# Kernel tuning notes

Measured on AMD Instinct MI355X. Metric: run time of the kernel, lower is better.

## Reference

```python
import jax, jax.numpy as jnp
import numpy as np

N_HEAD = 16
N_KV = 4
HEAD_DIM = 128
EPS = float(np.finfo(np.float32).eps)  # torch F.rms_norm default eps


def _rope_tables(T, half, dtype=jnp.float32):
    inv_freq = 1.0 / (10000.0 ** (jnp.arange(half, dtype=dtype) / half))
    ang = jnp.arange(T, dtype=dtype)[:, None] * inv_freq[None, :]  # (T, half)
    cos = jnp.cos(ang)[None, :, None, :]  # (1, T, 1, half)
    sin = jnp.sin(ang)[None, :, None, :]
    return cos, sin


def setup_inputs() -> dict:
    key = jax.random.key(0)
    ks = jax.random.split(key, 5)
    B, T, C = 2, 2048, 2048
    x = jax.random.normal(ks[0], (B, T, C), dtype=jnp.float32)
    cos, sin = _rope_tables(T, HEAD_DIM // 2)
    s = 0.02
    W_Q = jax.random.normal(ks[1], (C, N_HEAD * HEAD_DIM), dtype=jnp.float32) * s
    W_K = jax.random.normal(ks[2], (C, N_KV * HEAD_DIM), dtype=jnp.float32) * s
    W_V = jax.random.normal(ks[3], (C, N_KV * HEAD_DIM), dtype=jnp.float32) * s
    W_O = jax.random.normal(ks[4], (C, C), dtype=jnp.float32) * s
    return {"x": x, "cos": cos, "sin": sin, "W_Q": W_Q, "W_K": W_K, "W_V": W_V, "W_O": W_O}


def _apply_rope(x, cos, sin):
    # x: (B,T,H,D); cos/sin: (1,T,1,D/2)
    d = x.shape[-1] // 2
    x1, x2 = x[..., :d], x[..., d:]
    return jnp.concatenate([x1 * cos + x2 * sin, -x1 * sin + x2 * cos], axis=-1)


def _rms_norm(x):
    return x * jax.lax.rsqrt(jnp.mean(x * x, axis=-1, keepdims=True) + EPS)


def reference(x, cos, sin, W_Q, W_K, W_V, W_O):
    B, T, C = x.shape
    G = N_HEAD // N_KV  # kv groups
    q = (x @ W_Q).reshape(B, T, N_HEAD, HEAD_DIM)
    k = (x @ W_K).reshape(B, T, N_KV, HEAD_DIM)
    v = (x @ W_V).reshape(B, T, N_KV, HEAD_DIM)
    q = _rms_norm(_apply_rope(q, cos[:, :T], sin[:, :T]))
    k = _rms_norm(_apply_rope(k, cos[:, :T], sin[:, :T]))
    # GQA: avoid materializing expanded K/V; group q by kv head
    qg = q.reshape(B, T, N_KV, G, HEAD_DIM)
    scale = 1.0 / jnp.sqrt(jnp.asarray(HEAD_DIM, dtype=x.dtype))
    scores = jnp.einsum("btkgd,bskd->bkgts", qg, k) * scale  # (B,Kv,G,T,T)
    causal = jnp.tril(jnp.ones((T, T), dtype=bool))
    scores = jnp.where(causal, scores, jnp.asarray(-jnp.inf, dtype=scores.dtype))
    attn = jax.nn.softmax(scores, axis=-1)
    out = jnp.einsum("bkgts,bskd->btkgd", attn, v).reshape(B, T, C)
    return out @ W_O
```

## Files before the change

kernel.cpp:

```cpp
#include <hip/hip_runtime.h>
#include <hip/hip_bf16.h>
#include <stdint.h>

typedef __bf16 bf16_4 __attribute__((ext_vector_type(4)));
typedef __bf16 bf16_8 __attribute__((ext_vector_type(8)));
typedef float f32x4 __attribute__((ext_vector_type(4)));

#define AS1 __attribute__((address_space(1)))
#define AS3 __attribute__((address_space(3)))

__device__ __forceinline__ void gload_lds16(const void* g, void* l) {
  __builtin_amdgcn_global_load_lds((const AS1 void*)g, (AS3 void*)l, 16, 0, 0);
}

__device__ __forceinline__ bool is_bf16_mode(const void* cosT) {
  return ((*reinterpret_cast<const uint32_t*>(cosT)) & 0xFFFFu) == 0x3F80u;
}

__global__ __launch_bounds__(256) void prep_all(const void* __restrict__ cosT,
                                                const void* __restrict__ sinT,
                                                const void* __restrict__ x,
                                                const void* __restrict__ WQ,
                                                const void* __restrict__ WK,
                                                const void* __restrict__ WV,
                                                const void* __restrict__ WO,
                                                float* __restrict__ csF,
                                                __bf16* __restrict__ xb,
                                                __bf16* __restrict__ Wt,
                                                __bf16* __restrict__ WOt) {
  const int blk = blockIdx.x, tid = threadIdx.x;
  const bool isb = is_bf16_mode(cosT);
  if (blk < 512) {
    const int i = blk * 256 + tid;
    if (isb) {
      csF[i]          = (float)reinterpret_cast<const __bf16*>(cosT)[i];
      csF[131072 + i] = (float)reinterpret_cast<const __bf16*>(sinT)[i];
    } else {
      csF[i]          = reinterpret_cast<const float*>(cosT)[i];
      csF[131072 + i] = reinterpret_cast<const float*>(sinT)[i];
    }
    return;
  }
  if (blk < 4608) {
    if (isb) return;
    const int i = (blk - 512) * 256 + tid;
    const float4* s = reinterpret_cast<const float4*>(x);
    const float4 a = s[2 * i], c = s[2 * i + 1];
    __bf16 o[8] = {(__bf16)a.x, (__bf16)a.y, (__bf16)a.z, (__bf16)a.w,
                   (__bf16)c.x, (__bf16)c.y, (__bf16)c.z, (__bf16)c.w};
    reinterpret_cast<int4*>(xb)[i] = *reinterpret_cast<int4*>(o);
    return;
  }
  __shared__ __bf16 t[64][33];
  const int tb = blk - 4608;
  const int bx = tb % 160, by = tb / 160;
  const void* src;
  __bf16* dst;
  int C, c0;
  if (bx < 64)      { src = WQ; dst = Wt;                        C = 2048; c0 = bx * 32; }
  else if (bx < 80) { src = WK; dst = Wt + (size_t)2048 * 2048;  C = 512;  c0 = (bx - 64) * 32; }
  else if (bx < 96) { src = WV; dst = Wt + (size_t)2560 * 2048;  C = 512;  c0 = (bx - 80) * 32; }
  else              { src = WO; dst = WOt;                       C = 2048; c0 = (bx - 96) * 32; }
  const int r0 = by * 64;
  {
    const int row = tid >> 2, cb = (tid & 3) * 8;
    bf16_8 v;
    if (isb) {
      v = *reinterpret_cast<const bf16_8*>(
          reinterpret_cast<const __bf16*>(src) + (size_t)(r0 + row) * C + c0 + cb);
    } else {
      const float* sp = reinterpret_cast<const float*>(src) + (size_t)(r0 + row) * C + c0 + cb;
      const float4 a = *reinterpret_cast<const float4*>(sp);
      const float4 b2 = *reinterpret_cast<const float4*>(sp + 4);
      v[0] = (__bf16)a.x;  v[1] = (__bf16)a.y;  v[2] = (__bf16)a.z;  v[3] = (__bf16)a.w;
      v[4] = (__bf16)b2.x; v[5] = (__bf16)b2.y; v[6] = (__bf16)b2.z; v[7] = (__bf16)b2.w;
    }
    #pragma unroll
    for (int k = 0; k < 8; ++k) t[row][cb + k] = v[k];
  }
  __syncthreads();
  {
    const int j = tid >> 3, seg = (tid & 7) * 8;
    bf16_8 v;
    #pragma unroll
    for (int k = 0; k < 8; ++k) v[k] = t[seg + k][j];
    *reinterpret_cast<bf16_8*>(dst + (size_t)(c0 + j) * 2048 + r0 + seg) = v;
  }
}

__global__ __launch_bounds__(512) void gemm8p(const __bf16* __restrict__ A,
                                              const __bf16* __restrict__ Bt,
                                              void* __restrict__ Cv,
                                              int M, int N, int K,
                                              const void* __restrict__ cosRaw) {
  __shared__ __attribute__((aligned(16))) __bf16 As[2][128 * 64];
  __shared__ __attribute__((aligned(16))) __bf16 Bs[2][256 * 64];
  const int tid = threadIdx.x;
  const int lane = tid & 63, w = tid >> 6;
  const int wm = w >> 2, wn = w & 3;
  const int r = lane & 15, g = lane >> 4;
  const int q8 = gridDim.x >> 3;
  const int wg = (blockIdx.x & 7) * q8 + (blockIdx.x >> 3);
  const int gx = M >> 7;
  const int bm = (wg % gx) * 128, bn = (wg / gx) * 256;
  const bool isb = is_bf16_mode(cosRaw);
  const int NT = K >> 6;

  f32x4 acc[4][4] = {};

#define STA(kt, p, j)                                                              \
  {                                                                                \
    const int o_ = tid * 16 + (j) * 8192;                                          \
    const int row_ = o_ >> 7, blk_ = (o_ >> 4) & 7;                                \
    gload_lds16(A + (size_t)(bm + row_) * K + (kt) * 64 + ((blk_ ^ (row_ & 7)) << 3), \
                (char*)As[p] + o_);                                                \
  }
#define STB(kt, p, j)                                                              \
  {                                                                                \
    const int o_ = tid * 16 + (j) * 8192;                                          \
    const int rl_ = o_ >> 7, blk_ = (o_ >> 4) & 7;                                 \
    const int gr_ = ((rl_ >> 5) & 3) * 64 + ((rl_ >> 7) & 1) * 32 + (rl_ & 31);    \
    gload_lds16(Bt + (size_t)(bn + gr_) * K + (kt) * 64 + ((blk_ ^ (rl_ & 7)) << 3), \
                (char*)Bs[p] + o_);                                                \
  }

  STA(0, 0, 0); STA(0, 0, 1);
  STB(0, 0, 0); STB(0, 0, 1); STB(0, 0, 2); STB(0, 0, 3);
  asm volatile("s_waitcnt vmcnt(2)\ns_barrier" ::: "memory");

  for (int kt = 0; kt < NT; ++kt) {
    const int cur = kt & 1, nxt = cur ^ 1;
    const bool pf = (kt + 1 < NT);
    const char* Ac = (const char*)As[cur];
    const char* Bc = (const char*)Bs[cur];

    bf16_8 af[4][2], bf[2][2];
    #pragma unroll
    for (int m = 0; m < 4; ++m)
      #pragma unroll
      for (int kk = 0; kk < 2; ++kk) {
        const int row = wm * 64 + m * 16 + r;
        af[m][kk] = *reinterpret_cast<const bf16_8*>(
            Ac + row * 128 + (((kk * 4 + g) ^ (row & 7)) << 4));
      }
    #pragma unroll
    for (int n = 0; n < 2; ++n)
      #pragma unroll
      for (int kk = 0; kk < 2; ++kk) {
        const int rl = wn * 32 + n * 16 + r;
        bf[n][kk] = *reinterpret_cast<const bf16_8*>(
            Bc + rl * 128 + (((kk * 4 + g) ^ (rl & 7)) << 4));
      }
    if (pf) { STA(kt + 1, nxt, 0); STA(kt + 1, nxt, 1); STB(kt + 1, nxt, 0); }
    __builtin_amdgcn_s_barrier();
    __builtin_amdgcn_s_setprio(1);
    #pragma unroll
    for (int kk = 0; kk < 2; ++kk)
      #pragma unroll
      for (int m = 0; m < 4; ++m)
        #pragma unroll
        for (int n = 0; n < 2; ++n)
          acc[m][n] = __builtin_amdgcn_mfma_f32_16x16x32_bf16(af[m][kk], bf[n][kk], acc[m][n], 0, 0, 0);
    __builtin_amdgcn_s_setprio(0);
    if (pf) asm volatile("s_waitcnt vmcnt(3)\ns_barrier" ::: "memory");
    else    asm volatile("s_waitcnt vmcnt(0)\ns_barrier" ::: "memory");

    bf16_8 bg[2][2];
    #pragma unroll
    for (int n = 0; n < 2; ++n)
      #pragma unroll
      for (int kk = 0; kk < 2; ++kk) {
        const int rl = 128 + wn * 32 + n * 16 + r;
        bg[n][kk] = *reinterpret_cast<const bf16_8*>(
            Bc + rl * 128 + (((kk * 4 + g) ^ (rl & 7)) << 4));
      }
    if (pf) { STB(kt + 1, nxt, 1); STB(kt + 1, nxt, 2); STB(kt + 1, nxt, 3); }
    __builtin_amdgcn_s_barrier();
    __builtin_amdgcn_s_setprio(1);
    #pragma unroll
    for (int kk = 0; kk < 2; ++kk)
      #pragma unroll
      for (int m = 0; m < 4; ++m)
        #pragma unroll
        for (int n = 0; n < 2; ++n)
          acc[m][n + 2] = __builtin_amdgcn_mfma_f32_16x16x32_bf16(af[m][kk], bg[n][kk], acc[m][n + 2], 0, 0, 0);
    __builtin_amdgcn_s_setprio(0);
    if (pf) asm volatile("s_waitcnt vmcnt(2)\ns_barrier" ::: "memory");
    else    asm volatile("s_waitcnt vmcnt(0)\ns_barrier" ::: "memory");
  }
#undef STA
#undef STB

  #pragma unroll
  for (int m = 0; m < 4; ++m)
    #pragma unroll
    for (int n = 0; n < 4; ++n)
      #pragma unroll
      for (int j = 0; j < 4; ++j) {
        const int row = bm + wm * 64 + m * 16 + g * 4 + j;
        const int col = bn + wn * 64 + n * 16 + r;
        const float v = acc[m][n][j];
        if (isb) reinterpret_cast<__bf16*>(Cv)[(size_t)row * N + col] = (__bf16)v;
        else     reinterpret_cast<float*>(Cv)[(size_t)row * N + col] = v;
      }
}

__global__ __launch_bounds__(512) void gemm8p3(const __bf16* __restrict__ Acvt,
                                               const void* __restrict__ Araw,
                                               const __bf16* __restrict__ Bt,
                                               __bf16* __restrict__ Cv,
                                               __bf16* __restrict__ vtOut,
                                               int M, int N, int K,
                                               const void* __restrict__ cosRaw) {
  __shared__ __attribute__((aligned(16))) __bf16 As[2][128 * 64];
  __shared__ __attribute__((aligned(16))) __bf16 Bs[2][384 * 64];
  const int tid = threadIdx.x;
  const int lane = tid & 63, w = tid >> 6;
  const int wm = w >> 2, wn = w & 3;
  const int r = lane & 15, g = lane >> 4;
  const int q8 = gridDim.x >> 3;
  const int wg = (blockIdx.x & 7) * q8 + (blockIdx.x >> 3);
  const int gx = M >> 7;
  const int bm = (wg % gx) * 128, bn = (wg / gx) * 384;
  const int NT = K >> 6;
  const bool isb = is_bf16_mode(cosRaw);
  const __bf16* A = isb ? (const __bf16*)Araw : Acvt;

  f32x4 acc[4][6] = {};

#define STA3(kt, p, j)                                                             \
  {                                                                                \
    const int o_ = tid * 16 + (j) * 8192;                                          \
    const int row_ = o_ >> 7, blk_ = (o_ >> 4) & 7;                                \
    gload_lds16(A + (size_t)(bm + row_) * K + (kt) * 64 + ((blk_ ^ (row_ & 7)) << 3), \
                (char*)As[p] + o_);                                                \
  }
#define STB3(kt, p, j)                                                             \
  {                                                                                \
    const int o_ = tid * 16 + (j) * 8192;                                          \
    const int rl_ = o_ >> 7, blk_ = (o_ >> 4) & 7;                                 \
    const int gr_ = ((rl_ & 127) >> 5) * 96 + (rl_ >> 7) * 32 + (rl_ & 31);        \
    gload_lds16(Bt + (size_t)(bn + gr_) * K + (kt) * 64 + ((blk_ ^ (rl_ & 7)) << 3), \
                (char*)Bs[p] + o_);                                                \
  }

  STA3(0, 0, 0); STA3(0, 0, 1);
  STB3(0, 0, 0); STB3(0, 0, 1); STB3(0, 0, 2);
  STB3(0, 0, 3); STB3(0, 0, 4); STB3(0, 0, 5);
  asm volatile("s_waitcnt vmcnt(4)\ns_barrier" ::: "memory");

  for (int kt = 0; kt < NT; ++kt) {
    const int cur = kt & 1, nxt = cur ^ 1;
    const bool pf = (kt + 1 < NT);
    const char* Ac = (const char*)As[cur];
    const char* Bc = (const char*)Bs[cur];
    bf16_8 af[4][2];

    {
      #pragma unroll
      for (int m = 0; m < 4; ++m)
        #pragma unroll
        for (int kk = 0; kk < 2; ++kk) {
          const int row = wm * 64 + m * 16 + r;
          af[m][kk] = *reinterpret_cast<const bf16_8*>(
              Ac + row * 128 + (((kk * 4 + g) ^ (row & 7)) << 4));
        }
      bf16_8 bf[2][2];
      #pragma unroll
      for (int n = 0; n < 2; ++n)
        #pragma unroll
        for (int kk = 0; kk < 2; ++kk) {
          const int rl = wn * 32 + n * 16 + r;
          bf[n][kk] = *reinterpret_cast<const bf16_8*>(
              Bc + rl * 128 + (((kk * 4 + g) ^ (r & 7)) << 4));
        }
      if (pf) { STA3(kt + 1, nxt, 0); STA3(kt + 1, nxt, 1); STB3(kt + 1, nxt, 0); }
      __builtin_amdgcn_s_barrier();
      __builtin_amdgcn_s_setprio(1);
      #pragma unroll
      for (int kk = 0; kk < 2; ++kk)
        #pragma unroll
        for (int m = 0; m < 4; ++m)
          #pragma unroll
          for (int n = 0; n < 2; ++n)
            acc[m][n] = __builtin_amdgcn_mfma_f32_16x16x32_bf16(af[m][kk], bf[n][kk], acc[m][n], 0, 0, 0);
      __builtin_amdgcn_s_setprio(0);
      if (pf) asm volatile("s_waitcnt vmcnt(5)\ns_barrier" ::: "memory");
      else    asm volatile("s_waitcnt vmcnt(0)\ns_barrier" ::: "memory");
    }

    {
      bf16_8 bf[2][2];
      #pragma unroll
      for (int n = 0; n < 2; ++n)
        #pragma unroll
        for (int kk = 0; kk < 2; ++kk) {
          const int rl = 128 + wn * 32 + n * 16 + r;
          bf[n][kk] = *reinterpret_cast<const bf16_8*>(
              Bc + rl * 128 + (((kk * 4 + g) ^ (r & 7)) << 4));
        }
      if (pf) { STB3(kt + 1, nxt, 1); STB3(kt + 1, nxt, 2); }
      __builtin_amdgcn_s_barrier();
      __builtin_amdgcn_s_setprio(1);
      #pragma unroll
      for (int kk = 0; kk < 2; ++kk)
        #pragma unroll
        for (int m = 0; m < 4; ++m)
          #pragma unroll
          for (int n = 0; n < 2; ++n)
            acc[m][n + 2] = __builtin_amdgcn_mfma_f32_16x16x32_bf16(af[m][kk], bf[n][kk], acc[m][n + 2], 0, 0, 0);
      __builtin_amdgcn_s_setprio(0);
      if (pf) asm volatile("s_waitcnt vmcnt(5)\ns_barrier" ::: "memory");
      else    asm volatile("s_waitcnt vmcnt(0)\ns_barrier" ::: "memory");
    }

    {
      bf16_8 bf[2][2];
      #pragma unroll
      for (int n = 0; n < 2; ++n)
        #pragma unroll
        for (int kk = 0; kk < 2; ++kk) {
          const int rl = 256 + wn * 32 + n * 16 + r;
          bf[n][kk] = *reinterpret_cast<const bf16_8*>(
              Bc + rl * 128 + (((kk * 4 + g) ^ (r & 7)) << 4));
        }
      if (pf) { STB3(kt + 1, nxt, 3); STB3(kt + 1, nxt, 4); STB3(kt + 1, nxt, 5); }
      __builtin_amdgcn_s_barrier();
      __builtin_amdgcn_s_setprio(1);
      #pragma unroll
      for (int kk = 0; kk < 2; ++kk)
        #pragma unroll
        for (int m = 0; m < 4; ++m)
          #pragma unroll
          for (int n = 0; n < 2; ++n)
            acc[m][n + 4] = __builtin_amdgcn_mfma_f32_16x16x32_bf16(af[m][kk], bf[n][kk], acc[m][n + 4], 0, 0, 0);
      __builtin_amdgcn_s_setprio(0);
      if (pf) asm volatile("s_waitcnt vmcnt(4)\ns_barrier" ::: "memory");
      else    asm volatile("s_waitcnt vmcnt(0)\ns_barrier" ::: "memory");
    }
  }
#undef STA3
#undef STB3

  #pragma unroll
  for (int m = 0; m < 4; ++m)
    #pragma unroll
    for (int n = 0; n < 6; ++n) {
      const int row0 = bm + wm * 64 + m * 16 + g * 4;
      const int col  = bn + wn * 96 + n * 16 + r;
      if (isb && col >= 2560) {
        const int vcol = col - 2560;
        const int bb = row0 >> 11;
        const int t0 = row0 & 2047;
        bf16_4 pk;
        #pragma unroll
        for (int j = 0; j < 4; ++j) pk[j] = (__bf16)acc[m][n][j];
        *reinterpret_cast<bf16_4*>(
            &vtOut[((size_t)bb * 512 + vcol) * 2048 + t0]) = pk;
      } else {
        #pragma unroll
        for (int j = 0; j < 4; ++j)
          Cv[(size_t)(row0 + j) * N + col] = (__bf16)acc[m][n][j];
      }
    }
}

__global__ __launch_bounds__(256) void rope_vtrans(__bf16* __restrict__ qkv,
                                                   const float* __restrict__ csF,
                                                   __bf16* __restrict__ vt,
                                                   const void* __restrict__ cosRaw) {
  const int blk = blockIdx.x, tid = threadIdx.x;
  if (blk < 4096) {
    const int gw = blk * 4 + (tid >> 6);
    const int lane = tid & 63;
    const int head = 16 + (gw & 3);
    const int m = gw >> 2;
    const int t = m & 2047;
    __bf16* p = qkv + (size_t)m * 3072 + head * 128;
    const float x1 = (float)p[lane];
    const float x2 = (float)p[lane + 64];
    const float c = csF[t * 64 + lane];
    const float s = csF[131072 + t * 64 + lane];
    const float y1 = x1 * c + x2 * s;
    const float y2 = x2 * c - x1 * s;
    float ss = y1 * y1 + y2 * y2;
    #pragma unroll
    for (int mk = 32; mk >= 1; mk >>= 1) ss += __shfl_xor(ss, mk, 64);
    const float inv = rsqrtf(ss * (1.0f / 128.0f) + 1.1920929e-7f);
    p[lane] = (__bf16)(y1 * inv);
    p[lane + 64] = (__bf16)(y2 * inv);
    return;
  }
  if (is_bf16_mode(cosRaw)) return;
  __shared__ __bf16 t[32][33];
  const int vb = blk - 4096;
  const int z = vb >> 10, rem = vb & 1023;
  const int x = rem & 63, y = rem >> 6;
  const int tx = tid & 31, ty = tid >> 5;
  const int t0 = x * 32, c0 = y * 32;
  #pragma unroll
  for (int i = 0; i < 32; i += 8)
    t[ty + i][tx] = qkv[(size_t)(z * 2048 + t0 + ty + i) * 3072 + 2560 + c0 + tx];
  __syncthreads();
  #pragma unroll
  for (int i = 0; i < 32; i += 8)
    vt[(size_t)(z * 512 + c0 + ty + i) * 2048 + t0 + tx] = t[tx][ty + i];
}

__global__ __launch_bounds__(256) void attn_fwd7(const __bf16* __restrict__ qkv,
                                                 const __bf16* __restrict__ vt,
                                                 __bf16* __restrict__ out,
                                                 const float* __restrict__ csF,
                                                 const void* __restrict__ cosRawT,
                                                 const void* __restrict__ sinRawT) {
  __shared__ __attribute__((aligned(16))) __bf16 Kl[64 * 128];
  __shared__ __attribute__((aligned(16))) __bf16 Vl[128 * 64];
  __shared__ __attribute__((aligned(16))) __bf16 Pl[4][16][64];

  const int tid = threadIdx.x, lane = tid & 63, w = tid >> 6;
  const int r = lane & 15, g = lane >> 4;
  const int lid = blockIdx.x;
  const int grp = lid & 7, inner = lid >> 3;
  const int b = grp >> 2, kvh = grp & 3;
  const int h = kvh * 4 + (inner & 3);
  const int qt = 31 - (inner >> 2);
  const int qpos = qt * 64 + w * 16 + r;
  const __bf16* Kbase = qkv + (size_t)(b * 2048) * 3072 + 2048 + kvh * 128;
  const __bf16* Vbase = vt + (size_t)((b * 4 + kvh) * 128) * 2048;

#define STAGE(kt)                                                               \
  {                                                                             \
    _Pragma("unroll")                                                           \
    for (int i_ = 0; i_ < 4; ++i_) {                                            \
      const int o_ = tid * 16 + i_ * 4096;                                      \
      const int krow_ = o_ >> 8;                                                \
      const int jj_ = (o_ >> 4) & 15;                                           \
      const int gj_ = (jj_ & 8) | ((jj_ ^ krow_) & 7);                          \
      gload_lds16(Kbase + (size_t)((kt) * 64 + krow_) * 3072 + gj_ * 8,         \
                  (char*)Kl + o_);                                              \
      const int d_ = o_ >> 7;                                                   \
      const int j2_ = (o_ >> 4) & 7;                                            \
      const int g2_ = j2_ ^ (d_ & 7);                                           \
      gload_lds16(Vbase + (size_t)d_ * 2048 + (kt) * 64 + g2_ * 8,              \
                  (char*)Vl + o_);                                              \
    }                                                                           \
  }

#define ATTN_TILE(kt, MASKED)                                                   \
  {                                                                             \
    STAGE(kt);                                                                  \
    asm volatile("s_waitcnt vmcnt(0)" ::: "memory");                            \
    __syncthreads();                                                            \
    f32x4 sacc[4] = {};                                                         \
    _Pragma("unroll")                                                           \
    for (int kb = 0; kb < 4; ++kb) {                                            \
      const int jj = kb * 4 + g;                                                \
      const int jp = (jj & 8) | ((jj ^ (r & 7)) & 7);                           \
      _Pragma("unroll")                                                         \
      for (int n = 0; n < 4; ++n) {                                             \
        const bf16_8 kf = *reinterpret_cast<const bf16_8*>(                     \
            (char*)Kl + (n * 16 + r) * 256 + jp * 16);                          \
        sacc[n] = __builtin_amdgcn_mfma_f32_16x16x32_bf16(kf, qf[kb], sacc[n], 0, 0, 0); \
      }                                                                         \
    }                                                                           \
    float p[4][4];                                                              \
    float pm = -1e30f;                                                          \
    _Pragma("unroll")                                                           \
    for (int n = 0; n < 4; ++n)                                                 \
      _Pragma("unroll")                                                         \
      for (int j = 0; j < 4; ++j) {                                             \
        float sv = sacc[n][j];                                                  \
        if (MASKED && ((kt) * 64 + n * 16 + g * 4 + j > qpos)) sv = -1e30f;     \
        p[n][j] = sv;                                                           \
        pm = fmaxf(pm, sv);                                                     \
      }                                                                         \
    pm = fmaxf(pm, __shfl_xor(pm, 16, 64));                                     \
    pm = fmaxf(pm, __shfl_xor(pm, 32, 64));                                     \
    float mn = mst;                                                             \
    if (!__all(pm - mst <= 12.0f)) {                                            \
      mn = fmaxf(mst, pm);                                                      \
      const float alpha = exp2f(mst - mn);                                      \
      mst = mn;                                                                 \
      lst *= alpha;                                                             \
      float av[4];                                                              \
      _Pragma("unroll")                                                         \
      for (int j = 0; j < 4; ++j) av[j] = __shfl(alpha, g * 4 + j, 64);         \
      _Pragma("unroll")                                                         \
      for (int dt = 0; dt < 8; ++dt)                                            \
        _Pragma("unroll")                                                       \
        for (int j = 0; j < 4; ++j) accO[dt][j] *= av[j];                       \
    }                                                                           \
    float rs = 0.0f;                                                            \
    _Pragma("unroll")                                                           \
    for (int n = 0; n < 4; ++n)                                                 \
      _Pragma("unroll")                                                         \
      for (int j = 0; j < 4; ++j) {                                             \
        p[n][j] = exp2f(p[n][j] - mn);                                          \
        rs += p[n][j];                                                          \
      }                                                                         \
    rs += __shfl_xor(rs, 16, 64);                                               \
    rs += __shfl_xor(rs, 32, 64);                                               \
    lst += rs;                                                                  \
    _Pragma("unroll")                                                           \
    for (int n = 0; n < 4; ++n) {                                               \
      bf16_4 pk;                                                                \
      _Pragma("unroll")                                                         \
      for (int j = 0; j < 4; ++j) pk[j] = (__bf16)p[n][j];                      \
      const int blk = 2 * n + (g >> 1);                                         \
      char* pw = plw + r * 128 + ((blk ^ (r & 7)) << 4) + (g & 1) * 8;          \
      *reinterpret_cast<bf16_4*>(pw) = pk;                                      \
    }                                                                           \
    _Pragma("unroll")                                                           \
    for (int half = 0; half < 2; ++half) {                                      \
      const bf16_8 pa = *reinterpret_cast<const bf16_8*>(                       \
          plw + r * 128 + (((half * 4 + g) ^ (r & 7)) << 4));                   \
      _Pragma("unroll")                                                         \
      for (int dt = 0; dt < 8; ++dt) {                                          \
        const int d = dt * 16 + r;                                              \
        const bf16_8 vf = *reinterpret_cast<const bf16_8*>(                     \
            (char*)Vl + d * 128 + ((half * 4 + g) ^ (d & 7)) * 16);             \
        accO[dt] = __builtin_amdgcn_mfma_f32_16x16x32_bf16(pa, vf, accO[dt], 0, 0, 0); \
      }                                                                         \
    }                                                                           \
    __syncthreads();                                                            \
  }

  bf16_8 qf[4];
  {
    const int trow = qt * 64 + w * 16 + r;
    const __bf16* qp = qkv + (size_t)(b * 2048 + trow) * 3072 + h * 128 + g * 8;
    bf16_8 rq[4];
    #pragma unroll
    for (int kb = 0; kb < 4; ++kb) rq[kb] = *reinterpret_cast<const bf16_8*>(qp + kb * 32);
    float cv[16], sv[16];
    if (is_bf16_mode(cosRawT)) {
      const __bf16* cb = reinterpret_cast<const __bf16*>(cosRawT) + (size_t)trow * 64 + g * 8;
      const __bf16* sb = reinterpret_cast<const __bf16*>(sinRawT) + (size_t)trow * 64 + g * 8;
      const bf16_8 clo = *reinterpret_cast<const bf16_8*>(cb);
      const bf16_8 chi = *reinterpret_cast<const bf16_8*>(cb + 32);
      const bf16_8 slo = *reinterpret_cast<const bf16_8*>(sb);
      const bf16_8 shi = *reinterpret_cast<const bf16_8*>(sb + 32);
      #pragma unroll
      for (int i = 0; i < 8; ++i) {
        cv[i] = (float)clo[i];  cv[8 + i] = (float)chi[i];
        sv[i] = (float)slo[i];  sv[8 + i] = (float)shi[i];
      }
    } else {
      const float* cb = csF + (size_t)trow * 64 + g * 8;
      const float* sb = csF + 131072 + (size_t)trow * 64 + g * 8;
      #pragma unroll
      for (int i = 0; i < 2; ++i) {
        const float4 c0 = *reinterpret_cast<const float4*>(cb + i * 4);
        const float4 c1 = *reinterpret_cast<const float4*>(cb + 32 + i * 4);
        const float4 s0 = *reinterpret_cast<const float4*>(sb + i * 4);
        const float4 s1 = *reinterpret_cast<const float4*>(sb + 32 + i * 4);
        cv[i * 4 + 0] = c0.x; cv[i * 4 + 1] = c0.y; cv[i * 4 + 2] = c0.z; cv[i * 4 + 3] = c0.w;
        cv[8 + i * 4 + 0] = c1.x; cv[8 + i * 4 + 1] = c1.y; cv[8 + i * 4 + 2] = c1.z; cv[8 + i * 4 + 3] = c1.w;
        sv[i * 4 + 0] = s0.x; sv[i * 4 + 1] = s0.y; sv[i * 4 + 2] = s0.z; sv[i * 4 + 3] = s0.w;
        sv[8 + i * 4 + 0] = s1.x; sv[8 + i * 4 + 1] = s1.y; sv[8 + i * 4 + 2] = s1.z; sv[8 + i * 4 + 3] = s1.w;
      }
    }
    float y[4][8];
    float ss = 0.0f;
    #pragma unroll
    for (int i = 0; i < 8; ++i) {
      const float c0 = cv[i],     s0 = sv[i];
      const float c1 = cv[8 + i], s1 = sv[8 + i];
      const float xa0 = (float)rq[0][i], xb0 = (float)rq[2][i];
      const float xa1 = (float)rq[1][i], xb1 = (float)rq[3][i];
      y[0][i] = xa0 * c0 + xb0 * s0;
      y[2][i] = xb0 * c0 - xa0 * s0;
      y[1][i] = xa1 * c1 + xb1 * s1;
      y[3][i] = xb1 * c1 - xa1 * s1;
      ss += y[0][i] * y[0][i] + y[1][i] * y[1][i] + y[2][i] * y[2][i] + y[3][i] * y[3][i];
    }
    ss += __shfl_xor(ss, 16, 64);
    ss += __shfl_xor(ss, 32, 64);
    const float inv = rsqrtf(ss * (1.0f / 128.0f) + 1.1920929e-7f) * 0.12751743f;
    #pragma unroll
    for (int kb = 0; kb < 4; ++kb)
      #pragma unroll
      for (int i = 0; i < 8; ++i) qf[kb][i] = (__bf16)(y[kb][i] * inv);
  }

  char* const plw = (char*)Pl + w * 2048;
  f32x4 accO[8] = {};
  float mst = -1e30f, lst = 0.0f;

  for (int kt = 0; kt < qt; ++kt) ATTN_TILE(kt, false);
  ATTN_TILE(qt, true);

  float lv[4];
  #pragma unroll
  for (int j = 0; j < 4; ++j) lv[j] = 1.0f / __shfl(lst, g * 4 + j, 64);
  #pragma unroll
  for (int dt = 0; dt < 8; ++dt)
    #pragma unroll
    for (int j = 0; j < 4; ++j) {
      const int t = qt * 64 + w * 16 + g * 4 + j;
      out[(size_t)(b * 2048 + t) * 2048 + h * 128 + dt * 16 + r] = (__bf16)(accO[dt][j] * lv[j]);
    }
#undef ATTN_TILE
#undef STAGE
}

extern "C" void kernel_launch(void* const* d_in, const int* in_sizes, int n_in,
                              void* d_out, int out_size, void* d_ws, size_t ws_size,
                              hipStream_t stream) {
  const void* x    = d_in[0];
  const void* cosT = d_in[1];
  const void* sinT = d_in[2];
  const void* W_Q  = d_in[3];
  const void* W_K  = d_in[4];
  const void* W_V  = d_in[5];
  const void* W_O  = d_in[6];

  const int B = 2, T = 2048, C = 2048;
  const int M = B * T;
  const int NQKV = 3072;

  char* ws = (char*)d_ws;
  ws += 256;
  float*  csF  = (float*)ws;                     ws += (size_t)2 * 131072 * 4;
  __bf16* xb   = (__bf16*)ws;                    ws += (size_t)M * C * 2;
  __bf16* Wt   = (__bf16*)ws;                    ws += (size_t)NQKV * C * 2;
  __bf16* WOt  = (__bf16*)ws;                    ws += (size_t)C * C * 2;
  __bf16* QKV  = (__bf16*)ws;                    ws += (size_t)M * NQKV * 2;
  __bf16* AO   = (__bf16*)ws;                    ws += (size_t)M * C * 2;
  __bf16* VT   = xb;

  prep_all<<<dim3(9728), 256, 0, stream>>>(cosT, sinT, x, W_Q, W_K, W_V, W_O,
                                           csF, xb, Wt, WOt);
  gemm8p3<<<dim3((M / 128) * (NQKV / 384)), 512, 0, stream>>>(xb, x, Wt, QKV, VT, M, NQKV, C, cosT);
  rope_vtrans<<<dim3(6144), 256, 0, stream>>>(QKV, csF, VT, cosT);
  attn_fwd7<<<dim3(1024), 256, 0, stream>>>(QKV, VT, AO, csF, cosT, sinT);
  gemm8p<<<dim3((M / 128) * (C / 256)), 512, 0, stream>>>(AO, WOt, d_out, M, C, C, cosT);
}
```

Measured before the change: 194.2 us.

## Double-buffer K/V tiles in attention to overlap global loads with compute

The attention kernel now keeps two LDS buffers for the K and V tiles. It issues the asynchronous global-to-LDS load for tile kt+1 before computing tile kt, and uses a partial vmcnt wait plus raw barriers instead of a full drain and __syncthreads each iteration. The goal is to hide global memory latency behind the MFMA and softmax work. In exchange, LDS use roughly doubles (about 72KB per block), which may lower occupancy, and correctness now depends on the hand-written waitcnt and barrier ordering.

```diff
diff --git a/kernel.cpp b/kernel.cpp
--- a/kernel.cpp
+++ b/kernel.cpp
@@ -407,14 +407,14 @@
     vt[(size_t)(z * 512 + c0 + ty + i) * 2048 + t0 + tx] = t[tx][ty + i];
 }
 
-__global__ __launch_bounds__(256) void attn_fwd7(const __bf16* __restrict__ qkv,
+__global__ __launch_bounds__(256) void attn_fwd9(const __bf16* __restrict__ qkv,
                                                  const __bf16* __restrict__ vt,
                                                  __bf16* __restrict__ out,
                                                  const float* __restrict__ csF,
                                                  const void* __restrict__ cosRawT,
                                                  const void* __restrict__ sinRawT) {
-  __shared__ __attribute__((aligned(16))) __bf16 Kl[64 * 128];
-  __shared__ __attribute__((aligned(16))) __bf16 Vl[128 * 64];
+  __shared__ __attribute__((aligned(16))) __bf16 Kl[2][64 * 128];
+  __shared__ __attribute__((aligned(16))) __bf16 Vl[2][128 * 64];
   __shared__ __attribute__((aligned(16))) __bf16 Pl[4][16][64];
 
   const int tid = threadIdx.x, lane = tid & 63, w = tid >> 6;
@@ -428,7 +428,7 @@
   const __bf16* Kbase = qkv + (size_t)(b * 2048) * 3072 + 2048 + kvh * 128;
   const __bf16* Vbase = vt + (size_t)((b * 4 + kvh) * 128) * 2048;
 
-#define STAGE(kt)                                                               \
+#define STAGE(kt, p)                                                            \
   {                                                                             \
     _Pragma("unroll")                                                           \
     for (int i_ = 0; i_ < 4; ++i_) {                                            \
@@ -437,20 +437,19 @@
       const int jj_ = (o_ >> 4) & 15;                                           \
       const int gj_ = (jj_ & 8) | ((jj_ ^ krow_) & 7);                          \
       gload_lds16(Kbase + (size_t)((kt) * 64 + krow_) * 3072 + gj_ * 8,         \
-                  (char*)Kl + o_);                                              \
+                  (char*)Kl[p] + o_);                                           \
       const int d_ = o_ >> 7;                                                   \
       const int j2_ = (o_ >> 4) & 7;                                            \
       const int g2_ = j2_ ^ (d_ & 7);                                           \
       gload_lds16(Vbase + (size_t)d_ * 2048 + (kt) * 64 + g2_ * 8,              \
-                  (char*)Vl + o_);                                              \
+                  (char*)Vl[p] + o_);                                           \
     }                                                                           \
   }
 
-#define ATTN_TILE(kt, MASKED)                                                   \
+#define ATTN_TILE(kt, p, MASKED)                                                \
   {                                                                             \
-    STAGE(kt);                                                                  \
-    asm volatile("s_waitcnt vmcnt(0)" ::: "memory");                            \
-    __syncthreads();                                                            \
+    const char* Kc = (const char*)Kl[p];                                        \
+    const char* Vc = (const char*)Vl[p];                                        \
     f32x4 sacc[4] = {};                                                         \
     _Pragma("unroll")                                                           \
     for (int kb = 0; kb < 4; ++kb) {                                            \
@@ -459,11 +458,11 @@
       _Pragma("unroll")                                                         \
       for (int n = 0; n < 4; ++n) {                                             \
         const bf16_8 kf = *reinterpret_cast<const bf16_8*>(                     \
-            (char*)Kl + (n * 16 + r) * 256 + jp * 16);                          \
+            Kc + (n * 16 + r) * 256 + jp * 16);                                 \
         sacc[n] = __builtin_amdgcn_mfma_f32_16x16x32_bf16(kf, qf[kb], sacc[n], 0, 0, 0); \
       }                                                                         \
     }                                                                           \
-    float p[4][4];                                                              \
+    float p_[4][4];                                                             \
     float pm = -1e30f;                                                          \
     _Pragma("unroll")                                                           \
     for (int n = 0; n < 4; ++n)                                                 \
@@ -471,7 +470,7 @@
       for (int j = 0; j < 4; ++j) {                                             \
         float sv = sacc[n][j];                                                  \
         if (MASKED && ((kt) * 64 + n * 16 + g * 4 + j > qpos)) sv = -1e30f;     \
-        p[n][j] = sv;                                                           \
+        p_[n][j] = sv;                                                          \
         pm = fmaxf(pm, sv);                                                     \
       }                                                                         \
     pm = fmaxf(pm, __shfl_xor(pm, 16, 64));                                     \
@@ -495,8 +494,8 @@
     for (int n = 0; n < 4; ++n)                                                 \
       _Pragma("unroll")                                                         \
       for (int j = 0; j < 4; ++j) {                                             \
-        p[n][j] = exp2f(p[n][j] - mn);                                          \
-        rs += p[n][j];                                                          \
+        p_[n][j] = exp2f(p_[n][j] - mn);                                        \
+        rs += p_[n][j];                                                         \
       }                                                                         \
     rs += __shfl_xor(rs, 16, 64);                                               \
     rs += __shfl_xor(rs, 32, 64);                                               \
@@ -505,7 +504,7 @@
     for (int n = 0; n < 4; ++n) {                                               \
       bf16_4 pk;                                                                \
       _Pragma("unroll")                                                         \
-      for (int j = 0; j < 4; ++j) pk[j] = (__bf16)p[n][j];                      \
+      for (int j = 0; j < 4; ++j) pk[j] = (__bf16)p_[n][j];                     \
       const int blk = 2 * n + (g >> 1);                                         \
       char* pw = plw + r * 128 + ((blk ^ (r & 7)) << 4) + (g & 1) * 8;          \
       *reinterpret_cast<bf16_4*>(pw) = pk;                                      \
@@ -518,11 +517,10 @@
       for (int dt = 0; dt < 8; ++dt) {                                          \
         const int d = dt * 16 + r;                                              \
         const bf16_8 vf = *reinterpret_cast<const bf16_8*>(                     \
-            (char*)Vl + d * 128 + ((half * 4 + g) ^ (d & 7)) * 16);             \
+            Vc + d * 128 + ((half * 4 + g) ^ (d & 7)) * 16);                    \
         accO[dt] = __builtin_amdgcn_mfma_f32_16x16x32_bf16(pa, vf, accO[dt], 0, 0, 0); \
       }                                                                         \
     }                                                                           \
-    __syncthreads();                                                            \
   }
 
   bf16_8 qf[4];
@@ -587,8 +585,22 @@
   f32x4 accO[8] = {};
   float mst = -1e30f, lst = 0.0f;
 
-  for (int kt = 0; kt < qt; ++kt) ATTN_TILE(kt, false);
-  ATTN_TILE(qt, true);
+  STAGE(0, 0);
+  for (int kt = 0; kt < qt; ++kt) {
+    const int cur = kt & 1;
+    asm volatile("s_barrier" ::: "memory");
+    STAGE(kt + 1, cur ^ 1);
+    asm volatile("s_waitcnt vmcnt(8)" ::: "memory");
+    asm volatile("s_barrier" ::: "memory");
+    ATTN_TILE(kt, cur, false);
+  }
+  {
+    const int cur = qt & 1;
+    asm volatile("s_barrier" ::: "memory");
+    asm volatile("s_waitcnt vmcnt(0)" ::: "memory");
+    asm volatile("s_barrier" ::: "memory");
+    ATTN_TILE(qt, cur, true);
+  }
 
   float lv[4];
   #pragma unroll
@@ -633,6 +645,6 @@
                                            csF, xb, Wt, WOt);
   gemm8p3<<<dim3((M / 128) * (NQKV / 384)), 512, 0, stream>>>(xb, x, Wt, QKV, VT, M, NQKV, C, cosT);
   rope_vtrans<<<dim3(6144), 256, 0, stream>>>(QKV, csF, VT, cosT);
-  attn_fwd7<<<dim3(1024), 256, 0, stream>>>(QKV, VT, AO, csF, cosT, sinT);
+  attn_fwd9<<<dim3(1024), 256, 0, stream>>>(QKV, VT, AO, csF, cosT, sinT);
   gemm8p<<<dim3((M / 128) * (C / 256)), 512, 0, stream>>>(AO, WOt, d_out, M, C, C, cosT);
 }
```

New measurement: 194.4 us (median of 3 runs). About the same (+0.1%).

## Process two query sub-tiles per wave in attention to reuse K/V fragments

Applied to the files above, without the earlier changes.

The attention kernel now runs 2 waves per block instead of 4, and each wave handles 32 query rows as two 16-row sub-tiles. Each K and V fragment loaded from LDS is used for two MFMAs, which halves LDS reads per unit of compute, and the staging loop is doubled to cover the tile with fewer threads. The cost is roughly double the accumulator and Q registers per wave, which may lower occupancy, and fewer waves per block to hide the K/V staging latency.

```diff
diff --git a/kernel.cpp b/kernel.cpp
--- a/kernel.cpp
+++ b/kernel.cpp
@@ -407,15 +407,15 @@
     vt[(size_t)(z * 512 + c0 + ty + i) * 2048 + t0 + tx] = t[tx][ty + i];
 }
 
-__global__ __launch_bounds__(256) void attn_fwd7(const __bf16* __restrict__ qkv,
-                                                 const __bf16* __restrict__ vt,
-                                                 __bf16* __restrict__ out,
-                                                 const float* __restrict__ csF,
-                                                 const void* __restrict__ cosRawT,
-                                                 const void* __restrict__ sinRawT) {
+__global__ __launch_bounds__(128) void attn_fwd10(const __bf16* __restrict__ qkv,
+                                                  const __bf16* __restrict__ vt,
+                                                  __bf16* __restrict__ out,
+                                                  const float* __restrict__ csF,
+                                                  const void* __restrict__ cosRawT,
+                                                  const void* __restrict__ sinRawT) {
   __shared__ __attribute__((aligned(16))) __bf16 Kl[64 * 128];
   __shared__ __attribute__((aligned(16))) __bf16 Vl[128 * 64];
-  __shared__ __attribute__((aligned(16))) __bf16 Pl[4][16][64];
+  __shared__ __attribute__((aligned(16))) __bf16 Pl[2][2][16][64];
 
   const int tid = threadIdx.x, lane = tid & 63, w = tid >> 6;
   const int r = lane & 15, g = lane >> 4;
@@ -424,15 +424,14 @@
   const int b = grp >> 2, kvh = grp & 3;
   const int h = kvh * 4 + (inner & 3);
   const int qt = 31 - (inner >> 2);
-  const int qpos = qt * 64 + w * 16 + r;
   const __bf16* Kbase = qkv + (size_t)(b * 2048) * 3072 + 2048 + kvh * 128;
   const __bf16* Vbase = vt + (size_t)((b * 4 + kvh) * 128) * 2048;
 
 #define STAGE(kt)                                                               \
   {                                                                             \
     _Pragma("unroll")                                                           \
-    for (int i_ = 0; i_ < 4; ++i_) {                                            \
-      const int o_ = tid * 16 + i_ * 4096;                                      \
+    for (int i_ = 0; i_ < 8; ++i_) {                                            \
+      const int o_ = tid * 16 + i_ * 2048;                                      \
       const int krow_ = o_ >> 8;                                                \
       const int jj_ = (o_ >> 4) & 15;                                           \
       const int gj_ = (jj_ & 8) | ((jj_ ^ krow_) & 7);                          \
@@ -451,7 +450,7 @@
     STAGE(kt);                                                                  \
     asm volatile("s_waitcnt vmcnt(0)" ::: "memory");                            \
     __syncthreads();                                                            \
-    f32x4 sacc[4] = {};                                                         \
+    f32x4 sacc[2][4] = {};                                                      \
     _Pragma("unroll")                                                           \
     for (int kb = 0; kb < 4; ++kb) {                                            \
       const int jj = kb * 4 + g;                                                \
@@ -460,74 +459,84 @@
       for (int n = 0; n < 4; ++n) {                                             \
         const bf16_8 kf = *reinterpret_cast<const bf16_8*>(                     \
             (char*)Kl + (n * 16 + r) * 256 + jp * 16);                          \
-        sacc[n] = __builtin_amdgcn_mfma_f32_16x16x32_bf16(kf, qf[kb], sacc[n], 0, 0, 0); \
+        sacc[0][n] = __builtin_amdgcn_mfma_f32_16x16x32_bf16(kf, qf[0][kb], sacc[0][n], 0, 0, 0); \
+        sacc[1][n] = __builtin_amdgcn_mfma_f32_16x16x32_bf16(kf, qf[1][kb], sacc[1][n], 0, 0, 0); \
       }                                                                         \
     }                                                                           \
-    float p[4][4];                                                              \
-    float pm = -1e30f;                                                          \
     _Pragma("unroll")                                                           \
-    for (int n = 0; n < 4; ++n)                                                 \
+    for (int m2 = 0; m2 < 2; ++m2) {                                            \
+      const int qpos = qt * 64 + w * 32 + m2 * 16 + r;                          \
+      float p_[4][4];                                                           \
+      float pm = -1e30f;                                                        \
       _Pragma("unroll")                                                         \
-      for (int j = 0; j < 4; ++j) {                                             \
-        float sv = sacc[n][j];                                                  \
-        if (MASKED && ((kt) * 64 + n * 16 + g * 4 + j > qpos)) sv = -1e30f;     \
-        p[n][j] = sv;                                                           \
-        pm = fmaxf(pm, sv);                                                     \
+      for (int n = 0; n < 4; ++n)                                               \
+        _Pragma("unroll")                                                       \
+        for (int j = 0; j < 4; ++j) {                                           \
+          float sv = sacc[m2][n][j];                                            \
+          if (MASKED && ((kt) * 64 + n * 16 + g * 4 + j > qpos)) sv = -1e30f;   \
+          p_[n][j] = sv;                                                        \
+          pm = fmaxf(pm, sv);                                                   \
+        }                                                                       \
+      pm = fmaxf(pm, __shfl_xor(pm, 16, 64));                                   \
+      pm = fmaxf(pm, __shfl_xor(pm, 32, 64));                                   \
+      float mn = mst[m2];                                                       \
+      if (!__all(pm - mst[m2] <= 12.0f)) {                                      \
+        mn = fmaxf(mst[m2], pm);                                                \
+        const float alpha = exp2f(mst[m2] - mn);                                \
+        mst[m2] = mn;                                                           \
+        lst[m2] *= alpha;                                                       \
+        float av[4];                                                            \
+        _Pragma("unroll")                                                       \
+        for (int j = 0; j < 4; ++j) av[j] = __shfl(alpha, g * 4 + j, 64);       \
+        _Pragma("unroll")                                                       \
+        for (int dt = 0; dt < 8; ++dt)                                          \
+          _Pragma("unroll")                                                     \
+          for (int j = 0; j < 4; ++j) accO[m2][dt][j] *= av[j];                 \
       }                                                                         \
-    pm = fmaxf(pm, __shfl_xor(pm, 16, 64));                                     \
-    pm = fmaxf(pm, __shfl_xor(pm, 32, 64));                                     \
-    float mn = mst;                                                             \
-    if (!__all(pm - mst <= 12.0f)) {                                            \
-      mn = fmaxf(mst, pm);                                                      \
-      const float alpha = exp2f(mst - mn);                                      \
-      mst = mn;                                                                 \
-      lst *= alpha;                                                             \
-      float av[4];                                                              \
+      float rs = 0.0f;                                                          \
       _Pragma("unroll")                                                         \
-      for (int j = 0; j < 4; ++j) av[j] = __shfl(alpha, g * 4 + j, 64);         \
+      for (int n = 0; n < 4; ++n)                                               \
+        _Pragma("unroll")                                                       \
+        for (int j = 0; j < 4; ++j) {                                           \
+          p_[n][j] = exp2f(p_[n][j] - mn);                                      \
+          rs += p_[n][j];                                                       \
+        }                                                                       \
+      rs += __shfl_xor(rs, 16, 64);                                             \
+      rs += __shfl_xor(rs, 32, 64);                                             \
+      lst[m2] += rs;                                                            \
+      char* const plw = (char*)Pl + (w * 2 + m2) * 2048;                        \
       _Pragma("unroll")                                                         \
-      for (int dt = 0; dt < 8; ++dt)                                            \
+      for (int n = 0; n < 4; ++n) {                                             \
+        bf16_4 pk;                                                              \
         _Pragma("unroll")                                                       \
-        for (int j = 0; j < 4; ++j) accO[dt][j] *= av[j];                       \
-    }                                                                           \
-    float rs = 0.0f;                                                            \
-    _Pragma("unroll")                                                           \
-    for (int n = 0; n < 4; ++n)                                                 \
-      _Pragma("unroll")                                                         \
-      for (int j = 0; j < 4; ++j) {                                             \
-        p[n][j] = exp2f(p[n][j] - mn);                                          \
-        rs += p[n][j];                                                          \
+        for (int j = 0; j < 4; ++j) pk[j] = (__bf16)p_[n][j];                   \
+        const int blk = 2 * n + (g >> 1);                                       \
+        char* pw = plw + r * 128 + ((blk ^ (r & 7)) << 4) + (g & 1) * 8;        \
+        *reinterpret_cast<bf16_4*>(pw) = pk;                                    \
       }                                                                         \
-    rs += __shfl_xor(rs, 16, 64);                                               \
-    rs += __shfl_xor(rs, 32, 64);                                               \
-    lst += rs;                                                                  \
-    _Pragma("unroll")                                                           \
-    for (int n = 0; n < 4; ++n) {                                               \
-      bf16_4 pk;                                                                \
-      _Pragma("unroll")                                                         \
-      for (int j = 0; j < 4; ++j) pk[j] = (__bf16)p[n][j];                      \
-      const int blk = 2 * n + (g >> 1);                                         \
-      char* pw = plw + r * 128 + ((blk ^ (r & 7)) << 4) + (g & 1) * 8;          \
-      *reinterpret_cast<bf16_4*>(pw) = pk;                                      \
     }                                                                           \
     _Pragma("unroll")                                                           \
     for (int half = 0; half < 2; ++half) {                                      \
-      const bf16_8 pa = *reinterpret_cast<const bf16_8*>(                       \
-          plw + r * 128 + (((half * 4 + g) ^ (r & 7)) << 4));                   \
+      const bf16_8 pa0 = *reinterpret_cast<const bf16_8*>(                      \
+          (char*)Pl + (w * 2 + 0) * 2048 + r * 128 + (((half * 4 + g) ^ (r & 7)) << 4)); \
+      const bf16_8 pa1 = *reinterpret_cast<const bf16_8*>(                      \
+          (char*)Pl + (w * 2 + 1) * 2048 + r * 128 + (((half * 4 + g) ^ (r & 7)) << 4)); \
       _Pragma("unroll")                                                         \
       for (int dt = 0; dt < 8; ++dt) {                                          \
         const int d = dt * 16 + r;                                              \
         const bf16_8 vf = *reinterpret_cast<const bf16_8*>(                     \
             (char*)Vl + d * 128 + ((half * 4 + g) ^ (d & 7)) * 16);             \
-        accO[dt] = __builtin_amdgcn_mfma_f32_16x16x32_bf16(pa, vf, accO[dt], 0, 0, 0); \
+        accO[0][dt] = __builtin_amdgcn_mfma_f32_16x16x32_bf16(pa0, vf, accO[0][dt], 0, 0, 0); \
+        accO[1][dt] = __builtin_amdgcn_mfma_f32_16x16x32_bf16(pa1, vf, accO[1][dt], 0, 0, 0); \
       }                                                                         \
     }                                                                           \
     __syncthreads();                                                            \
   }
 
-  bf16_8 qf[4];
-  {
-    const int trow = qt * 64 + w * 16 + r;
+  bf16_8 qf[2][4];
+  #pragma unroll
+  for (int m2 = 0; m2 < 2; ++m2) {
+    const int trow = qt * 64 + w * 32 + m2 * 16 + r;
     const __bf16* qp = qkv + (size_t)(b * 2048 + trow) * 3072 + h * 128 + g * 8;
     bf16_8 rq[4];
     #pragma unroll
@@ -580,26 +589,29 @@
     #pragma unroll
     for (int kb = 0; kb < 4; ++kb)
       #pragma unroll
-      for (int i = 0; i < 8; ++i) qf[kb][i] = (__bf16)(y[kb][i] * inv);
-  }
-
-  char* const plw = (char*)Pl + w * 2048;
-  f32x4 accO[8] = {};
-  float mst = -1e30f, lst = 0.0f;
+      for (int i = 0; i < 8; ++i) qf[m2][kb][i] = (__bf16)(y[kb][i] * inv);
+  }
+
+  f32x4 accO[2][8] = {};
+  float mst[2] = {-1e30f, -1e30f}, lst[2] = {0.0f, 0.0f};
 
   for (int kt = 0; kt < qt; ++kt) ATTN_TILE(kt, false);
   ATTN_TILE(qt, true);
 
-  float lv[4];
   #pragma unroll
-  for (int j = 0; j < 4; ++j) lv[j] = 1.0f / __shfl(lst, g * 4 + j, 64);
-  #pragma unroll
-  for (int dt = 0; dt < 8; ++dt)
-    #pragma unroll
-    for (int j = 0; j < 4; ++j) {
-      const int t = qt * 64 + w * 16 + g * 4 + j;
-      out[(size_t)(b * 2048 + t) * 2048 + h * 128 + dt * 16 + r] = (__bf16)(accO[dt][j] * lv[j]);
-    }
+  for (int m2 = 0; m2 < 2; ++m2) {
+    float lv[4];
+    #pragma unroll
+    for (int j = 0; j < 4; ++j) lv[j] = 1.0f / __shfl(lst[m2], g * 4 + j, 64);
+    #pragma unroll
+    for (int dt = 0; dt < 8; ++dt)
+      #pragma unroll
+      for (int j = 0; j < 4; ++j) {
+        const int t = qt * 64 + w * 32 + m2 * 16 + g * 4 + j;
+        out[(size_t)(b * 2048 + t) * 2048 + h * 128 + dt * 16 + r] =
+            (__bf16)(accO[m2][dt][j] * lv[j]);
+      }
+  }
 #undef ATTN_TILE
 #undef STAGE
 }
@@ -633,6 +645,6 @@
                                            csF, xb, Wt, WOt);
   gemm8p3<<<dim3((M / 128) * (NQKV / 384)), 512, 0, stream>>>(xb, x, Wt, QKV, VT, M, NQKV, C, cosT);
   rope_vtrans<<<dim3(6144), 256, 0, stream>>>(QKV, csF, VT, cosT);
-  attn_fwd7<<<dim3(1024), 256, 0, stream>>>(QKV, VT, AO, csF, cosT, sinT);
+  attn_fwd10<<<dim3(1024), 128, 0, stream>>>(QKV, VT, AO, csF, cosT, sinT);
   gemm8p<<<dim3((M / 128) * (C / 256)), 512, 0, stream>>>(AO, WOt, d_out, M, C, C, cosT);
 }
```

Result: slower. 219.8 us (+13.1%).
